# Optimization experiments

Measured on AMD Instinct MI355X. Metric: run time of the kernel, lower is better.

## Reference

```python
import jax, jax.numpy as jnp
import numpy as np

IMG, PATCH, DIM, DEPTH, HEADS = 224, 16, 768, 12, 12
GRID = IMG // PATCH            # 14 patches per side
NPATCH = GRID * GRID           # 196
N = NPATCH + 1                 # 197 tokens incl. cls
HD = DIM // HEADS              # 64
NRD = (2 * GRID - 1) ** 2 + 3  # 732 relative-distance entries (incl. 3 cls slots)
FF = 4 * DIM                   # 3072
BATCH = 32


def _rel_pos_index():
    # Faithful port of the torch buffer construction (with_cls_token=True).
    coords = np.stack(np.meshgrid(np.arange(GRID), np.arange(GRID), indexing='ij'))
    cf = coords.reshape(2, -1)                                   # [2, 196]
    rel = (cf[:, :, None] - cf[:, None, :]).transpose(1, 2, 0)   # [196,196,2]
    rel = rel.astype(np.int64)
    rel[:, :, 0] += GRID - 1
    rel[:, :, 1] += GRID - 1
    rel[:, :, 0] *= 2 * GRID - 1
    rpi = np.zeros((N, N), dtype=np.int32)
    rpi[1:, 1:] = rel.sum(-1)
    rpi[0, :] = NRD - 3
    rpi[:, 0] = NRD - 2
    rpi[0, 0] = NRD - 1
    return jnp.asarray(rpi)

RPI = _rel_pos_index()  # [197,197] int32, constant


def layernorm(x, w, b, eps=1e-5):
    mu = x.mean(-1, keepdims=True)
    var = x.var(-1, keepdims=True)  # biased, like torch LayerNorm
    return (x - mu) * jax.lax.rsqrt(var + eps) * w + b


def setup_inputs() -> dict:
    key = jax.random.key(0)
    ks = jax.random.split(key, 12)
    s = 0.02
    f32 = jnp.float32
    return {
        'x': jax.random.normal(ks[0], (BATCH, 3, IMG, IMG), f32),
        # PatchEmbed conv (stride == kernel) expressed as a matmul weight.
        'patch_w': jax.random.normal(ks[1], (DIM, 3 * PATCH * PATCH), f32) * s,
        'patch_b': jnp.zeros((DIM,), f32),
        'cls_token': jax.random.normal(ks[2], (1, 1, DIM), f32) * s,
        # Per-block params, stacked along depth for lax.scan.
        'norm1_w': jnp.ones((DEPTH, DIM), f32),
        'norm1_b': jnp.zeros((DEPTH, DIM), f32),
        'qkv_w': jax.random.normal(ks[3], (DEPTH, 3 * DIM, DIM), f32) * s,
        'q_bias': jax.random.normal(ks[4], (DEPTH, DIM), f32) * s,
        'v_bias': jax.random.normal(ks[5], (DEPTH, DIM), f32) * s,
        'rpb_table': jax.random.normal(ks[6], (DEPTH, NRD, HEADS), f32) * s,
        'proj_w': jax.random.normal(ks[7], (DEPTH, DIM, DIM), f32) * s,
        'proj_b': jnp.zeros((DEPTH, DIM), f32),
        'norm2_w': jnp.ones((DEPTH, DIM), f32),
        'norm2_b': jnp.zeros((DEPTH, DIM), f32),
        'fc1_w': jax.random.normal(ks[8], (DEPTH, FF, DIM), f32) * s,
        'fc1_b': jnp.zeros((DEPTH, FF), f32),
        'fc2_w': jax.random.normal(ks[9], (DEPTH, DIM, FF), f32) * s,
        'fc2_b': jnp.zeros((DEPTH, DIM), f32),
        'normf_w': jnp.ones((DIM,), f32),
        'normf_b': jnp.zeros((DIM,), f32),
    }


def reference(x, patch_w, patch_b, cls_token, norm1_w, norm1_b, qkv_w, q_bias, v_bias,
              rpb_table, proj_w, proj_b, norm2_w, norm2_b, fc1_w, fc1_b, fc2_w, fc2_b,
              normf_w, normf_b):
    B = x.shape[0]
    # Patch embed: stride==kernel conv == patchify + matmul.
    p = x.reshape(B, 3, GRID, PATCH, GRID, PATCH).transpose(0, 2, 4, 1, 3, 5)
    p = p.reshape(B, NPATCH, 3 * PATCH * PATCH)
    tokens = p @ patch_w.T + patch_b                              # [B,196,768]
    tokens = jnp.concatenate([jnp.broadcast_to(cls_token, (B, 1, DIM)), tokens], axis=1)
    scale = HD ** -0.5

    def block(h, params):
        (n1w, n1b, qw, qb, vb, rpt, pw, pb, n2w, n2b, f1w, f1b, f2w, f2b) = params
        y = layernorm(h, n1w, n1b)
        bias = jnp.concatenate([qb, jnp.zeros_like(vb), vb])      # k bias is zero
        qkv = (y @ qw.T + bias).reshape(B, N, 3, HEADS, HD).transpose(2, 0, 3, 1, 4)
        q, k, v = qkv[0] * scale, qkv[1], qkv[2]                  # [B,H,N,HD]
        attn = jnp.einsum('bhnd,bhmd->bhnm', q, k)                # [B,H,N,N]
        rpb = rpt[RPI]                                            # [N,N,H] gather
        attn = attn + rpb.transpose(2, 0, 1)[None]
        attn = jax.nn.softmax(attn, axis=-1)
        o = jnp.einsum('bhnm,bhmd->bnhd', attn, v).reshape(B, N, DIM)
        h = h + o @ pw.T + pb
        y = layernorm(h, n2w, n2b)
        y = jax.nn.gelu(y @ f1w.T + f1b, approximate=False)       # torch nn.GELU (erf)
        h = h + y @ f2w.T + f2b
        return h, None

    params = (norm1_w, norm1_b, qkv_w, q_bias, v_bias, rpb_table, proj_w, proj_b,
              norm2_w, norm2_b, fc1_w, fc1_b, fc2_w, fc2_b)
    tokens, _ = jax.lax.scan(block, tokens, params)
    return layernorm(tokens, normf_w, normf_b)                    # [B,197,768]
```

## Files before the change

### kernel.cpp

```cpp
#include <hip/hip_runtime.h>
#include <hip/hip_bf16.h>


#define B_     32
#define DIM_   768
#define N_     197
#define M_     (B_*N_)
#define NP_    196
#define MP_    (B_*NP_)
#define HEADS_ 12
#define HD_    64
#define FF_    3072
#define NRD_   732
#define QKV_   2304
#define DEPTH_ 12

typedef unsigned short u16;
typedef unsigned int   u32;
typedef __attribute__((ext_vector_type(4))) float    f32x4;
typedef __attribute__((ext_vector_type(8))) u16      ushort8;
typedef __attribute__((ext_vector_type(8))) __bf16   bf16x8;

__device__ __forceinline__ float b2f(u16 u) {
    return __builtin_bit_cast(float, ((u32)u) << 16);
}
__device__ __forceinline__ u16 f2b(float f) {
    u32 u = __builtin_bit_cast(u32, f);
    u32 r = u + 0x7fffu + ((u >> 16) & 1u);
    return (u16)(r >> 16);
}
__device__ __forceinline__ float lo16(u32 v) { return __builtin_bit_cast(float, v << 16); }
__device__ __forceinline__ float hi16(u32 v) { return __builtin_bit_cast(float, v & 0xffff0000u); }

__device__ __forceinline__ f32x4 mfma16(ushort8 a, ushort8 b, f32x4 c) {
    return __builtin_amdgcn_mfma_f32_16x16x32_bf16(
        __builtin_bit_cast(bf16x8, a), __builtin_bit_cast(bf16x8, b), c, 0, 0, 0);
}

__device__ __forceinline__ void gload16(const u16* g, u16* lds) {
    __builtin_amdgcn_global_load_lds(
        (const __attribute__((address_space(1))) void*)g,
        (__attribute__((address_space(3))) void*)lds, 16, 0, 0);
}

__global__ void cvt_k(const float* __restrict__ src, u16* __restrict__ dst, int n8) {
    int g = blockIdx.x * 256 + threadIdx.x;
    if (g >= n8) return;
    size_t o = (size_t)g * 8;
    float4 f0 = *(const float4*)(src + o);
    float4 f1 = *(const float4*)(src + o + 4);
    ushort8 r;
    r[0]=f2b(f0.x); r[1]=f2b(f0.y); r[2]=f2b(f0.z); r[3]=f2b(f0.w);
    r[4]=f2b(f1.x); r[5]=f2b(f1.y); r[6]=f2b(f1.z); r[7]=f2b(f1.w);
    *(ushort8*)(dst + o) = r;
}

#define SEG0 1769472
#define SEG1 589824
#define SEG2 2359296
#define SEG3 2359296
__global__ void cvt4_k(const float* __restrict__ s0, const float* __restrict__ s1,
                       const float* __restrict__ s2, const float* __restrict__ s3,
                       u16* __restrict__ dst) {
    int g = blockIdx.x * 256 + threadIdx.x;
    if (g >= (SEG0+SEG1+SEG2+SEG3)/8) return;
    size_t o = (size_t)g * 8;
    const float* src; size_t lo_;
    if (o < SEG0)             { src = s0; lo_ = o; }
    else if (o < SEG0+SEG1)   { src = s1; lo_ = o - SEG0; }
    else if (o < (size_t)SEG0+SEG1+SEG2) { src = s2; lo_ = o - SEG0 - SEG1; }
    else                      { src = s3; lo_ = o - SEG0 - SEG1 - SEG2; }
    float4 f0 = *(const float4*)(src + lo_);
    float4 f1 = *(const float4*)(src + lo_ + 4);
    ushort8 r;
    r[0]=f2b(f0.x); r[1]=f2b(f0.y); r[2]=f2b(f0.z); r[3]=f2b(f0.w);
    r[4]=f2b(f1.x); r[5]=f2b(f1.y); r[6]=f2b(f1.z); r[7]=f2b(f1.w);
    *(ushort8*)(dst + o) = r;
}

__global__ void patchify_k(const float* __restrict__ X, u16* __restrict__ P) {
    int idx = blockIdx.x * 256 + threadIdx.x;
    if (idx >= MP_ * DIM_) return;
    int row = idx / DIM_, k = idx - row * DIM_;
    int b = row / NP_, p = row - b * NP_;
    int gy = p / 14, gx = p - gy * 14;
    int c = k >> 8, r = k & 255;
    int py = r >> 4, px = r & 15;
    P[idx] = f2b(X[((b * 3 + c) * 224 + gy * 16 + py) * 224 + gx * 16 + px]);
}

__global__ void build_tokens_k(const float* __restrict__ P, const float* __restrict__ cls,
                               float* __restrict__ T) {
    int idx = blockIdx.x * 256 + threadIdx.x;
    if (idx >= M_ * DIM_) return;
    int row = idx / DIM_, c = idx - row * DIM_;
    int b = row / N_, t = row - b * N_;
    T[idx] = (t == 0) ? cls[c] : P[(size_t)(b * NP_ + t - 1) * DIM_ + c];
}

__global__ void qkvbias_all_k(const float* __restrict__ qb, const float* __restrict__ vb,
                              float* __restrict__ out) {
    int g = blockIdx.x * 256 + threadIdx.x;
    if (g >= DEPTH_ * QKV_) return;
    int l = g / QKV_, n = g - l * QKV_;
    out[g] = (n < DIM_) ? qb[l * DIM_ + n]
                        : (n < 2 * DIM_ ? 0.f : vb[l * DIM_ + n - 2 * DIM_]);
}

template <int OUTBF>
__global__ void layernorm_k(const float* __restrict__ X, const float* __restrict__ w,
                            const float* __restrict__ bta, void* __restrict__ Yv) {
    int row = blockIdx.x;
    const float* x = X + (size_t)row * DIM_;
    int t = threadIdx.x;
    float v[3]; float s = 0.f, q = 0.f;
#pragma unroll
    for (int i = 0; i < 3; i++) { float u = x[t + i * 256]; v[i] = u; s += u; q += u * u; }
#pragma unroll
    for (int off = 32; off > 0; off >>= 1) {
        s += __shfl_down(s, off, 64);
        q += __shfl_down(q, off, 64);
    }
    __shared__ float ss[4], qq[4];
    int wid = t >> 6, lane = t & 63;
    if (!lane) { ss[wid] = s; qq[wid] = q; }
    __syncthreads();
    s = ss[0] + ss[1] + ss[2] + ss[3];
    q = qq[0] + qq[1] + qq[2] + qq[3];
    float mu = s * (1.f / 768.f);
    float var = q * (1.f / 768.f) - mu * mu;
    float rs = rsqrtf(var + 1e-5f);
#pragma unroll
    for (int i = 0; i < 3; i++) {
        int c = t + i * 256;
        float o = (v[i] - mu) * rs * w[c] + bta[c];
        if (OUTBF) ((u16*)Yv)[(size_t)row * DIM_ + c] = f2b(o);
        else       ((float*)Yv)[(size_t)row * DIM_ + c] = o;
    }
}

template <int ACT, int OUTBF>
__launch_bounds__(512)
__global__ void gemm_bt(const u16* __restrict__ A, const u16* __restrict__ W,
                        const float* __restrict__ bias, const float* res,
                        void* Cv, int M, int Nc, int K) {
    __shared__ u16 As[4][128 * 32];
    __shared__ u16 Ws[4][128 * 32];
    const int tid = threadIdx.x;
    const int lane = tid & 63, w = tid >> 6;
    const int llo = lane & 15, lhi = lane >> 4;
    const int wm = w & 3, wn = w >> 2;

    const int nwg = gridDim.x * gridDim.y;
    int bid = blockIdx.y * gridDim.x + blockIdx.x;
    {
        int q = nwg >> 3, r = nwg & 7;
        int xcd = bid & 7, idx = bid >> 3;
        bid = (xcd < r ? xcd * (q + 1) : r * (q + 1) + (xcd - r) * q) + idx;
    }
    const int m0 = (bid / gridDim.x) * 128, n0 = (bid % gridDim.x) * 128;

    f32x4 acc[2][4] = {};

    const int srow = tid >> 2;
    const int scol = ((tid & 3) ^ ((srow >> 1) & 3)) * 8;
    int ar = m0 + srow; if (ar >= M) ar = M - 1;
    const u16* ga = A + (size_t)ar * K + scol;
    const u16* gw = W + (size_t)(n0 + srow) * K + scol;
    const int ldso = (w * 16) * 32;

    const int rslot = (lhi ^ ((llo >> 1) & 3)) * 8;

    const int nt = K >> 5;

#pragma unroll
    for (int p = 0; p < 3; ++p) {
        gload16(ga + p * 32, As[p] + ldso);
        gload16(gw + p * 32, Ws[p] + ldso);
    }

    for (int t = 0; t < nt; ++t) {
        if (t < nt - 2)      asm volatile("s_waitcnt vmcnt(4)" ::: "memory");
        else if (t < nt - 1) asm volatile("s_waitcnt vmcnt(2)" ::: "memory");
        else                 asm volatile("s_waitcnt vmcnt(0)" ::: "memory");
        __builtin_amdgcn_s_barrier();

        const u16* ab = As[t & 3];
        const u16* wb = Ws[t & 3];
        ushort8 af[2], bfr[4];
#pragma unroll
        for (int mi = 0; mi < 2; mi++)
            af[mi] = *(const ushort8*)(ab + (wm * 32 + mi * 16 + llo) * 32 + rslot);
#pragma unroll
        for (int ni = 0; ni < 4; ni++)
            bfr[ni] = *(const ushort8*)(wb + (wn * 64 + ni * 16 + llo) * 32 + rslot);
#pragma unroll
        for (int mi = 0; mi < 2; mi++)
#pragma unroll
            for (int ni = 0; ni < 4; ni++)
                acc[mi][ni] = mfma16(af[mi], bfr[ni], acc[mi][ni]);

        if (t + 3 < nt) {
            gload16(ga + (size_t)(t + 3) * 32, As[(t + 3) & 3] + ldso);
            gload16(gw + (size_t)(t + 3) * 32, Ws[(t + 3) & 3] + ldso);
        }
    }

    const int cb = n0 + wn * 64 + llo;
    const int rb = m0 + wm * 32 + lhi * 4;
#pragma unroll
    for (int ni = 0; ni < 4; ni++) {
        int col = cb + ni * 16;
        float bv = bias ? bias[col] : 0.f;
#pragma unroll
        for (int mi = 0; mi < 2; mi++) {
#pragma unroll
            for (int rg = 0; rg < 4; rg++) {
                int row = rb + mi * 16 + rg;
                if (row >= M) continue;
                float t = acc[mi][ni][rg] + bv;
                if (ACT) t = 0.5f * t * (1.f + erff(t * 0.70710678118654752f));
                if (res) t += res[(size_t)row * Nc + col];
                if (OUTBF) ((u16*)Cv)[(size_t)row * Nc + col] = f2b(t);
                else       ((float*)Cv)[(size_t)row * Nc + col] = t;
            }
        }
    }
}

__device__ __forceinline__ int vswz(int d) {
    return ((d & 7) ^ ((d >> 3) & 7)) << 3;
}

__launch_bounds__(256)
__global__ void attn3_k(const u16* __restrict__ qkv, const float* __restrict__ rpt,
                        u16* __restrict__ O) {
    __shared__ u16 smem[16128 + 16384];
    u16* Ks = smem;
    u16* Vt = smem + 16128;
    u16* Ps = smem;
    const int b = blockIdx.x / HEADS_, hh = blockIdx.x % HEADS_;
    const int i0 = blockIdx.y * 64;
    const int t = threadIdx.x;
    const int w = t >> 6, lane = t & 63;
    const int lhi = lane >> 4, llo = lane & 15;
    const size_t base = (size_t)b * N_ * QKV_ + (size_t)hh * HD_;
    const int iw = i0 + w * 16;

    int qrow = iw + llo; if (qrow > 196) qrow = 196;
    const ushort8 af0 = *(const ushort8*)(qkv + base + (size_t)qrow * QKV_ + lhi * 8);
    const ushort8 af1 = *(const ushort8*)(qkv + base + (size_t)qrow * QKV_ + 32 + lhi * 8);

    for (int g = t; g < 1576; g += 256) {
        int j = g >> 3, d0 = (g & 7) * 8;
        ushort8 kv = *(const ushort8*)(qkv + base + (size_t)j * QKV_ + 768 + d0);
        *(ushort8*)(Ks + j * 72 + d0) = kv;
        ushort8 vv = *(const ushort8*)(qkv + base + (size_t)j * QKV_ + 1536 + d0);
#pragma unroll
        for (int e = 0; e < 8; e++) {
            int d = d0 + e;
            Vt[d * 256 + (j ^ vswz(d))] = ((const u16*)&vv)[e];
        }
    }
    if (t < 216) {
        int j = 197 + (t >> 3), d0 = (t & 7) * 8;
        *(uint4*)(Ks + j * 72 + d0) = make_uint4(0u, 0u, 0u, 0u);
    }
    for (int g = t; g < 1728; g += 256) {
        int d = g / 27, c = 197 + (g - d * 27);
        Vt[d * 256 + (c ^ vswz(d))] = 0;
    }
    __syncthreads();

    const bool wvalid = (iw <= 196);
    f32x4 acc[14] = {};
    float mx[4], sum[4];

    if (wvalid) {
#pragma unroll
        for (int jt = 0; jt < 14; jt++) {
            const u16* kp = Ks + (jt * 16 + llo) * 72 + lhi * 8;
            ushort8 b0 = *(const ushort8*)(kp);
            ushort8 b1 = *(const ushort8*)(kp + 32);
            acc[jt] = mfma16(af0, b0, acc[jt]);
            acc[jt] = mfma16(af1, b1, acc[jt]);
        }
        int iy4[4], ix4[4]; bool icls[4];
#pragma unroll
        for (int rg = 0; rg < 4; rg++) {
            int i = iw + lhi * 4 + rg; if (i > 196) i = 196;
            icls[rg] = (i == 0);
            int pi = i - 1;
            iy4[rg] = pi / 14; ix4[rg] = pi - iy4[rg] * 14;
            mx[rg] = -INFINITY;
        }
#pragma unroll
        for (int jt = 0; jt < 14; jt++) {
            int j = jt * 16 + llo;
            if (j <= 196) {
                bool jcls = (j == 0);
                int pj = j - 1;
                int jy = pj / 14, jx = pj - jy * 14;
#pragma unroll
                for (int rg = 0; rg < 4; rg++) {
                    int idx;
                    if (icls[rg])  idx = jcls ? (NRD_ - 1) : (NRD_ - 3);
                    else if (jcls) idx = NRD_ - 2;
                    else           idx = (iy4[rg] - jy + 13) * 27 + (ix4[rg] - jx + 13);
                    float sv = acc[jt][rg] * 0.125f + rpt[idx * HEADS_ + hh];
                    acc[jt][rg] = sv;
                    mx[rg] = fmaxf(mx[rg], sv);
                }
            } else {
#pragma unroll
                for (int rg = 0; rg < 4; rg++) acc[jt][rg] = -INFINITY;
            }
        }
#pragma unroll
        for (int rg = 0; rg < 4; rg++) {
#pragma unroll
            for (int off = 1; off < 16; off <<= 1)
                mx[rg] = fmaxf(mx[rg], __shfl_xor(mx[rg], off, 64));
            sum[rg] = 0.f;
        }
#pragma unroll
        for (int jt = 0; jt < 14; jt++)
#pragma unroll
            for (int rg = 0; rg < 4; rg++) {
                float ev = __expf(acc[jt][rg] - mx[rg]);
                acc[jt][rg] = ev;
                sum[rg] += ev;
            }
#pragma unroll
        for (int rg = 0; rg < 4; rg++) {
#pragma unroll
            for (int off = 1; off < 16; off <<= 1)
                sum[rg] += __shfl_xor(sum[rg], off, 64);
            sum[rg] = 1.f / sum[rg];
        }
#pragma unroll
        for (int jt = 0; jt < 14; jt++)
#pragma unroll
            for (int rg = 0; rg < 4; rg++) acc[jt][rg] *= sum[rg];
    }
    __syncthreads();

    if (wvalid) {
#pragma unroll
        for (int jt = 0; jt < 14; jt++)
#pragma unroll
            for (int rg = 0; rg < 4; rg++)
                Ps[(w * 16 + lhi * 4 + rg) * 232 + jt * 16 + llo] = f2b(acc[jt][rg]);
        f32x4 o[4] = {};
#pragma unroll
        for (int jk = 0; jk < 7; jk++) {
            ushort8 pa = *(const ushort8*)(Ps + (w * 16 + llo) * 232 + jk * 32 + lhi * 8);
#pragma unroll
            for (int dt = 0; dt < 4; dt++) {
                int d = dt * 16 + llo;
                ushort8 vf = *(const ushort8*)(Vt + d * 256 + ((jk * 32 + lhi * 8) ^ vswz(d)));
                o[dt] = mfma16(pa, vf, o[dt]);
            }
        }
#pragma unroll
        for (int dt = 0; dt < 4; dt++)
#pragma unroll
            for (int rg = 0; rg < 4; rg++) {
                int i = iw + lhi * 4 + rg;
                if (i <= 196)
                    O[(size_t)(b * N_ + i) * DIM_ + hh * HD_ + dt * 16 + llo] = f2b(o[dt][rg]);
            }
    }
}

extern "C" void kernel_launch(void* const* d_in, const int* in_sizes, int n_in,
                              void* d_out, int out_size, void* d_ws, size_t ws_size,
                              hipStream_t stream) {
    (void)in_sizes; (void)n_in; (void)out_size; (void)ws_size;
    const float* x    = (const float*)d_in[0];
    const float* pew  = (const float*)d_in[1];
    const float* peb  = (const float*)d_in[2];
    const float* cls  = (const float*)d_in[3];
    const float* n1w  = (const float*)d_in[4];
    const float* n1b  = (const float*)d_in[5];
    const float* qkvw = (const float*)d_in[6];
    const float* qb   = (const float*)d_in[7];
    const float* vb   = (const float*)d_in[8];
    const float* rpt  = (const float*)d_in[9];
    const float* pw   = (const float*)d_in[10];
    const float* pb   = (const float*)d_in[11];
    const float* n2w  = (const float*)d_in[12];
    const float* n2b  = (const float*)d_in[13];
    const float* f1w  = (const float*)d_in[14];
    const float* f1b  = (const float*)d_in[15];
    const float* f2w  = (const float*)d_in[16];
    const float* f2b_ = (const float*)d_in[17];
    const float* nfw  = (const float*)d_in[18];
    const float* nfb  = (const float*)d_in[19];

    float* ws = (float*)d_ws;
    float* h     = ws;
    u16*   y     = (u16*)(ws + 4841472);
    float* un    = ws + 4841472 + 2420736;
    u16*   wbuf  = (u16*)(un + 9682944);
    float* qbias = (float*)(wbuf + 7077888);
    u16*   qkvb   = (u16*)un;
    u16*   hidden = (u16*)un;
    u16*   pmat   = (u16*)un;
    float* pout   = un + 4816896;

    const int MT = (M_ + 127) / 128;

    cvt_k<<<288, 256, 0, stream>>>(pew, wbuf, SEG1 / 8);
    patchify_k<<<(MP_ * DIM_ + 255) / 256, 256, 0, stream>>>(x, pmat);
    qkvbias_all_k<<<(DEPTH_ * QKV_ + 255) / 256, 256, 0, stream>>>(qb, vb, qbias);
    gemm_bt<0, 0><<<dim3(6, 49), 512, 0, stream>>>(pmat, wbuf, peb, nullptr, pout,
                                                   MP_, DIM_, DIM_);
    build_tokens_k<<<(M_ * DIM_ + 255) / 256, 256, 0, stream>>>(pout, cls, h);

    for (int l = 0; l < 12; l++) {
        layernorm_k<1><<<M_, 256, 0, stream>>>(h, n1w + l * DIM_, n1b + l * DIM_, y);
        cvt4_k<<<3456, 256, 0, stream>>>(qkvw + (size_t)l * SEG0, pw + (size_t)l * SEG1,
                                         f1w + (size_t)l * SEG2, f2w + (size_t)l * SEG3, wbuf);
        gemm_bt<0, 1><<<dim3(18, MT), 512, 0, stream>>>(y, wbuf, qbias + l * QKV_, nullptr,
                                                        qkvb, M_, QKV_, DIM_);
        attn3_k<<<dim3(384, 4), 256, 0, stream>>>(qkvb, rpt + (size_t)l * NRD_ * HEADS_, y);
        gemm_bt<0, 0><<<dim3(6, MT), 512, 0, stream>>>(y, wbuf + SEG0, pb + l * DIM_, h, h,
                                                       M_, DIM_, DIM_);
        layernorm_k<1><<<M_, 256, 0, stream>>>(h, n2w + l * DIM_, n2b + l * DIM_, y);
        gemm_bt<1, 1><<<dim3(24, MT), 512, 0, stream>>>(y, wbuf + SEG0 + SEG1, f1b + l * FF_,
                                                        nullptr, hidden, M_, FF_, DIM_);
        gemm_bt<0, 0><<<dim3(6, MT), 512, 0, stream>>>(hidden, wbuf + SEG0 + SEG1 + SEG2,
                                                       f2b_ + l * DIM_, h, h, M_, DIM_, FF_);
    }
    layernorm_k<0><<<M_, 256, 0, stream>>>(h, nfw, nfb, d_out);
}
```

Before: 3.447 ms.

## Stage GEMM epilogue through LDS for vectorized stores, triple-buffer K pipeline

The GEMM epilogue now writes accumulators to shared memory in two column halves and reads them back so each thread emits 16-byte vectorized stores with bias, residual and activation applied, in place of scattered scalar stores. The K-loop pipeline drops from four LDS stages to three, which frees shared memory, and launch bounds now request higher occupancy. Exact erf GELU is replaced with the Abramowitz-Stegun polynomial approximation (error around 1e-7). Wave-to-tile mapping changes (wn = w&1, wm = w>>1). The trade-offs are a shallower prefetch depth and extra barriers in the epilogue, and the bias pointer is now dereferenced without a null check.

Result: faster. 2.940 ms (-14.7%).

```diff
diff --git a/kernel.cpp b/kernel.cpp
--- a/kernel.cpp
+++ b/kernel.cpp
@@ -41,6 +41,17 @@
     __builtin_amdgcn_global_load_lds(
         (const __attribute__((address_space(1))) void*)g,
         (__attribute__((address_space(3))) void*)lds, 16, 0, 0);
+}
+
+__device__ __forceinline__ float gelu_f(float x) {
+    float z  = x * 0.70710678118654752f;
+    float az = fabsf(z);
+    float t  = 1.f / (1.f + 0.3275911f * az);
+    float p  = t * (0.254829592f + t * (-0.284496736f + t * (1.421413741f +
+               t * (-1.453152027f + t * 1.061405429f))));
+    float er = 1.f - p * __expf(-az * az);
+    er = __builtin_copysignf(er, z);
+    return 0.5f * x * (1.f + er);
 }
 
 __global__ void cvt_k(const float* __restrict__ src, u16* __restrict__ dst, int n8) {
@@ -140,16 +151,17 @@
 }
 
 template <int ACT, int OUTBF>
-__launch_bounds__(512)
+__launch_bounds__(512, 6)
 __global__ void gemm_bt(const u16* __restrict__ A, const u16* __restrict__ W,
                         const float* __restrict__ bias, const float* res,
                         void* Cv, int M, int Nc, int K) {
-    __shared__ u16 As[4][128 * 32];
-    __shared__ u16 Ws[4][128 * 32];
+    __shared__ __align__(16) u16 smem[6 * 4096];
+    u16* As = smem;
+    u16* Ws = smem + 3 * 4096;
     const int tid = threadIdx.x;
     const int lane = tid & 63, w = tid >> 6;
     const int llo = lane & 15, lhi = lane >> 4;
-    const int wm = w & 3, wn = w >> 2;
+    const int wn = w & 1, wm = w >> 1;
 
     const int nwg = gridDim.x * gridDim.y;
     int bid = blockIdx.y * gridDim.x + blockIdx.x;
@@ -173,20 +185,19 @@
 
     const int nt = K >> 5;
 
-#pragma unroll
-    for (int p = 0; p < 3; ++p) {
-        gload16(ga + p * 32, As[p] + ldso);
-        gload16(gw + p * 32, Ws[p] + ldso);
-    }
-
+    gload16(ga,      As + ldso);
+    gload16(gw,      Ws + ldso);
+    gload16(ga + 32, As + 4096 + ldso);
+    gload16(gw + 32, Ws + 4096 + ldso);
+
+    int cbuf = 0, sbuf = 2;
     for (int t = 0; t < nt; ++t) {
-        if (t < nt - 2)      asm volatile("s_waitcnt vmcnt(4)" ::: "memory");
-        else if (t < nt - 1) asm volatile("s_waitcnt vmcnt(2)" ::: "memory");
-        else                 asm volatile("s_waitcnt vmcnt(0)" ::: "memory");
+        if (t < nt - 1) asm volatile("s_waitcnt vmcnt(2)" ::: "memory");
+        else            asm volatile("s_waitcnt vmcnt(0)" ::: "memory");
         __builtin_amdgcn_s_barrier();
 
-        const u16* ab = As[t & 3];
-        const u16* wb = Ws[t & 3];
+        const u16* ab = As + cbuf * 4096;
+        const u16* wb = Ws + cbuf * 4096;
         ushort8 af[2], bfr[4];
 #pragma unroll
         for (int mi = 0; mi < 2; mi++)
@@ -200,31 +211,75 @@
             for (int ni = 0; ni < 4; ni++)
                 acc[mi][ni] = mfma16(af[mi], bfr[ni], acc[mi][ni]);
 
-        if (t + 3 < nt) {
-            gload16(ga + (size_t)(t + 3) * 32, As[(t + 3) & 3] + ldso);
-            gload16(gw + (size_t)(t + 3) * 32, Ws[(t + 3) & 3] + ldso);
-        }
-    }
-
-    const int cb = n0 + wn * 64 + llo;
-    const int rb = m0 + wm * 32 + lhi * 4;
-#pragma unroll
-    for (int ni = 0; ni < 4; ni++) {
-        int col = cb + ni * 16;
-        float bv = bias ? bias[col] : 0.f;
-#pragma unroll
-        for (int mi = 0; mi < 2; mi++) {
-#pragma unroll
-            for (int rg = 0; rg < 4; rg++) {
-                int row = rb + mi * 16 + rg;
-                if (row >= M) continue;
-                float t = acc[mi][ni][rg] + bv;
-                if (ACT) t = 0.5f * t * (1.f + erff(t * 0.70710678118654752f));
-                if (res) t += res[(size_t)row * Nc + col];
-                if (OUTBF) ((u16*)Cv)[(size_t)row * Nc + col] = f2b(t);
-                else       ((float*)Cv)[(size_t)row * Nc + col] = t;
-            }
-        }
+        if (t + 2 < nt) {
+            gload16(ga + (size_t)(t + 2) * 32, As + sbuf * 4096 + ldso);
+            gload16(gw + (size_t)(t + 2) * 32, Ws + sbuf * 4096 + ldso);
+        }
+        cbuf = (cbuf + 1 == 3) ? 0 : cbuf + 1;
+        sbuf = (sbuf + 1 == 3) ? 0 : sbuf + 1;
+    }
+
+    __syncthreads();
+    float* eb = (float*)smem;
+#pragma unroll
+    for (int half = 0; half < 2; ++half) {
+        if (wn == half) {
+#pragma unroll
+            for (int mi = 0; mi < 2; mi++)
+#pragma unroll
+                for (int ni = 0; ni < 4; ni++)
+#pragma unroll
+                    for (int rg = 0; rg < 4; rg++)
+                        eb[(wm * 32 + mi * 16 + lhi * 4 + rg) * 68 + ni * 16 + llo] =
+                            acc[mi][ni][rg];
+        }
+        __syncthreads();
+        if (OUTBF) {
+#pragma unroll
+            for (int i = 0; i < 2; ++i) {
+                int idx = tid + i * 512;
+                int row = idx >> 3, c8 = (idx & 7) * 8;
+                int grow = m0 + row, gcol = n0 + half * 64 + c8;
+                f32x4 v0 = *(const f32x4*)(eb + row * 68 + c8);
+                f32x4 v1 = *(const f32x4*)(eb + row * 68 + c8 + 4);
+                if (grow < M) {
+                    float4 b0 = *(const float4*)(bias + gcol);
+                    float4 b1 = *(const float4*)(bias + gcol + 4);
+                    float o0[4] = {v0[0]+b0.x, v0[1]+b0.y, v0[2]+b0.z, v0[3]+b0.w};
+                    float o1[4] = {v1[0]+b1.x, v1[1]+b1.y, v1[2]+b1.z, v1[3]+b1.w};
+                    ushort8 r;
+#pragma unroll
+                    for (int j = 0; j < 4; j++) {
+                        float a0 = ACT ? gelu_f(o0[j]) : o0[j];
+                        float a1 = ACT ? gelu_f(o1[j]) : o1[j];
+                        r[j] = f2b(a0); r[4 + j] = f2b(a1);
+                    }
+                    *(ushort8*)((u16*)Cv + (size_t)grow * Nc + gcol) = r;
+                }
+            }
+        } else {
+#pragma unroll
+            for (int i = 0; i < 4; ++i) {
+                int idx = tid + i * 512;
+                int row = idx >> 4, c4 = (idx & 15) * 4;
+                int grow = m0 + row, gcol = n0 + half * 64 + c4;
+                f32x4 v = *(const f32x4*)(eb + row * 68 + c4);
+                if (grow < M) {
+                    float4 bv = *(const float4*)(bias + gcol);
+                    float4 o;
+                    o.x = v[0] + bv.x; o.y = v[1] + bv.y;
+                    o.z = v[2] + bv.z; o.w = v[3] + bv.w;
+                    if (ACT) { o.x = gelu_f(o.x); o.y = gelu_f(o.y);
+                               o.z = gelu_f(o.z); o.w = gelu_f(o.w); }
+                    if (res) {
+                        float4 rv = *(const float4*)(res + (size_t)grow * Nc + gcol);
+                        o.x += rv.x; o.y += rv.y; o.z += rv.z; o.w += rv.w;
+                    }
+                    *(float4*)((float*)Cv + (size_t)grow * Nc + gcol) = o;
+                }
+            }
+        }
+        __syncthreads();
     }
 }
 
```
